# Kernel tuning notes

Hardware: AMD Instinct MI355X
Metric: run time of the kernel (lower is better)

Reference implementation:

```python
import jax, jax.numpy as jnp
import numpy as np

B = 1024      # batch
H = 512       # n_hidden
F = 32        # lstm_features
CIN = 4       # input channels
K = 30        # conv kernel
STRIDE = 6
L = 924       # input length -> T = (924-30)//6+1 = 150
KD = 40       # deconv kernel
NSTEPS = 10   # lstm_future_out
DN = ('NCH', 'OIH', 'NCH')


def setup_inputs() -> dict:
    key = jax.random.key(0)
    ks = jax.random.split(key, 14)
    s = 0.05
    rn = lambda k, shape: jax.random.normal(k, shape, jnp.float32) * s
    return dict(
        x=jax.random.normal(ks[0], (B, CIN, L), jnp.float32),
        conv_w=rn(ks[1], (F, CIN, K)), conv_b=rn(ks[2], (F,)),
        Wih0=rn(ks[3], (4 * H, F)), Whh0=rn(ks[4], (4 * H, H)),
        bih0=rn(ks[5], (4 * H,)), bhh0=rn(ks[6], (4 * H,)),
        Wih1=rn(ks[7], (4 * H, H)), Whh1=rn(ks[8], (4 * H, H)),
        bih1=rn(ks[9], (4 * H,)), bhh1=rn(ks[10], (4 * H,)),
        dec_w=rn(ks[11], (F, H)), dec_b=rn(ks[12], (F,)),
        deconv_w=rn(ks[13], (F, 1, KD)),
    )


def _cell(x, h, c, Wih, Whh, b):
    # PyTorch LSTM gate order: i, f, g, o
    g = x @ Wih.T + h @ Whh.T + b
    i, f, gg, o = jnp.split(g, 4, axis=-1)
    c = jax.nn.sigmoid(f) * c + jax.nn.sigmoid(i) * jnp.tanh(gg)
    h = jax.nn.sigmoid(o) * jnp.tanh(c)
    return h, c


def _lstm_layer(seq, Wih, Whh, b):
    # seq: [T, B, in] -> ys: [T, B, H], final (h, c)
    n = seq.shape[1]
    h0 = jnp.zeros((n, H), seq.dtype)
    c0 = jnp.zeros((n, H), seq.dtype)
    def step(carry, x):
        h, c = _cell(x, carry[0], carry[1], Wih, Whh, b)
        return (h, c), h
    (hT, cT), ys = jax.lax.scan(step, (h0, c0), seq)
    return ys, hT, cT


def _forward(x, conv_w, conv_b, Wih0, Whh0, bih0, bhh0,
             Wih1, Whh1, bih1, bhh1, dec_w, dec_b, deconv_w):
    # encoder conv: [B,4,L] -> [B,F,T]
    z = jax.lax.conv_general_dilated(x, conv_w, (STRIDE,), [(0, 0)],
                                     dimension_numbers=DN) + conv_b[None, :, None]
    z = jax.nn.relu(z)
    seq = jnp.transpose(z, (2, 0, 1))  # [T, B, F]
    b0, b1 = bih0 + bhh0, bih1 + bhh1
    s0, h0, c0 = _lstm_layer(seq, Wih0, Whh0, b0)
    s1, h1, c1 = _lstm_layer(s0, Wih1, Whh1, b1)
    out = s1 @ dec_w.T + dec_b                 # [T, B, F]
    y0 = out[-1]                               # output[-2:-1] of encoder -> last decoded step
    def dec_step(carry, _):
        y, ha, ca, hb, cb = carry
        ha, ca = _cell(y, ha, ca, Wih0, Whh0, b0)
        hb, cb = _cell(ha, hb, cb, Wih1, Whh1, b1)
        y = hb @ dec_w.T + dec_b
        return (y, ha, ca, hb, cb), y
    _, fut = jax.lax.scan(dec_step, (y0, h0, c0, h1, c1), None, length=NSTEPS)
    fut = jnp.transpose(fut, (1, 2, 0))        # [B, F, 10]
    # ConvTranspose1d (stride=1, pad=0, no bias) == cross-correlation with
    # spatially flipped, channel-swapped kernel on input padded by KD-1.
    kt = jnp.transpose(jnp.flip(deconv_w, -1), (1, 0, 2))  # [1, F, KD]
    return jax.lax.conv_general_dilated(fut, kt, (1,), [(KD - 1, KD - 1)],
                                        dimension_numbers=DN)  # [B, 1, 49]


def reference(x, conv_w, conv_b, Wih0, Whh0, bih0, bhh0,
              Wih1, Whh1, bih1, bhh1, dec_w, dec_b, deconv_w):
    return _forward(x, conv_w, conv_b, Wih0, Whh0, bih0, bhh0,
                    Wih1, Whh1, bih1, bhh1, dec_w, dec_b, deconv_w)
```

## Files before the change

kernel.cpp:

```cpp
#include <hip/hip_runtime.h>
#include <hip/hip_bf16.h>

typedef __hip_bfloat16 bf16;
typedef __attribute__((ext_vector_type(8))) short short8;
typedef __attribute__((ext_vector_type(4))) float float4v;

#define B_    1024
#define H_    512
#define G4H   2048
#define F_    32
#define CIN_  4
#define K_    30
#define STRIDE_ 6
#define L_    924
#define T_    150
#define KD_   40
#define NSTEPS_ 10
#define BH    (B_ * H_)

__device__ __forceinline__ float sigmoidf_(float x) { return 1.f / (1.f + __expf(-x)); }
__device__ __forceinline__ float tanhf_(float x)    { return 1.f - 2.f / (__expf(2.f * x) + 1.f); }
__device__ __forceinline__ float b2f_(short s) {
    return __uint_as_float(((unsigned)(unsigned short)s) << 16);
}
__device__ __forceinline__ void stwt_(bf16* p, float v) {
    union { __hip_bfloat16 b; unsigned short u; } cv;
    cv.b = __float2bfloat16(v);
    __hip_atomic_store((unsigned short*)p, cv.u, __ATOMIC_RELAXED, __HIP_MEMORY_SCOPE_AGENT);
}

__global__ __launch_bounds__(256) void cvt_kernel(const float* __restrict__ src,
                                                  bf16* __restrict__ dst, int n) {
    int i = blockIdx.x * 256 + threadIdx.x;
    if (i < n) dst[i] = __float2bfloat16(src[i]);
}

__global__ void bias_kernel(const float* __restrict__ bih0, const float* __restrict__ bhh0,
                            const float* __restrict__ bih1, const float* __restrict__ bhh1,
                            float* __restrict__ b0, float* __restrict__ b1) {
    int i = blockIdx.x * 256 + threadIdx.x;
    if (i < G4H)      b0[i] = bih0[i] + bhh0[i];
    else if (i < 2*G4H) { int j = i - G4H; b1[j] = bih1[j] + bhh1[j]; }
}

__global__ __launch_bounds__(256) void conv_kernel(
    const float* __restrict__ x, const float* __restrict__ w,
    const float* __restrict__ cb, bf16* __restrict__ seq)
{
    __shared__ float w_lds[CIN_ * K_ * F_];
    __shared__ float x_lds[CIN_ * L_];
    int tid = threadIdx.x;
    int b = blockIdx.x;
    for (int i = tid; i < CIN_ * K_ * F_; i += 256) {
        int f = i & 31, r = i >> 5;
        w_lds[r * 32 + f] = w[f * (CIN_ * K_) + r];
    }
    const float* xb = x + (size_t)b * (CIN_ * L_);
    for (int i = tid; i < CIN_ * L_; i += 256)
        x_lds[i] = xb[i];
    __syncthreads();
    int f = tid & 31, tt = tid >> 5;
    float cbf = cb[f];
    for (int t0 = 0; t0 < T_; t0 += 8) {
        int t = t0 + tt;
        if (t < T_) {
            float acc = cbf;
            #pragma unroll
            for (int c = 0; c < CIN_; ++c) {
                const float* xr = x_lds + c * L_ + t * STRIDE_;
                const float* wr = w_lds + c * K_ * 32 + f;
                #pragma unroll
                for (int k = 0; k < K_; ++k)
                    acc += xr[k] * wr[k * 32];
            }
            acc = fmaxf(acc, 0.f);
            seq[(size_t)t * (B_ * F_) + b * F_ + f] = __float2bfloat16(acc);
        }
    }
}

__device__ __forceinline__ void wait1(const int* fg, int tgt, bool inv) {
    if (tgt > 0) {
        if (threadIdx.x < 16) {
            const long long* p = (const long long*)fg + threadIdx.x;
            for (int n = 0; ; ++n) {
                long long v = __hip_atomic_load(p, __ATOMIC_RELAXED, __HIP_MEMORY_SCOPE_AGENT);
                int a = (int)v, b = (int)(v >> 32);
                if (__all(a >= tgt && b >= tgt)) break;
                if (n < 2) __builtin_amdgcn_s_sleep(2);
                else       __builtin_amdgcn_s_sleep(32);
            }
        }
        __syncthreads();
        if (inv) __builtin_amdgcn_fence(__ATOMIC_ACQUIRE, "agent");
    } else {
        __syncthreads();
    }
}

__device__ __forceinline__ void signal1(int* f, int val) {
    __syncthreads();
    if (threadIdx.x == 0) {
        __builtin_amdgcn_s_waitcnt(0);
        __hip_atomic_store(f, val, __ATOMIC_RELAXED, __HIP_MEMORY_SCOPE_AGENT);
    }
}

#define MFMA_ __builtin_amdgcn_mfma_f32_16x16x32_bf16
template<int NKS, int XSTR>
__device__ __forceinline__ void gemm_acc(
    const bf16* __restrict__ X, const short8* __restrict__ W,
    float4v (&acc)[4][4], int mrow, int quad, int lane)
{
    for (int ks = 0; ks < NKS; ++ks) {
        short8 av[4];
        #pragma unroll
        for (int ms = 0; ms < 4; ++ms)
            av[ms] = *(const short8*)(X + (size_t)(mrow + ms * 16) * XSTR
                                      + ks * 32 + quad * 8);
        #pragma unroll
        for (int g = 0; g < 4; ++g) {
            short8 bfr = W[(ks * 4 + g) * 64 + lane];
            #pragma unroll
            for (int ms = 0; ms < 4; ++ms)
                acc[ms][g] = MFMA_(av[ms], bfr, acc[ms][g], 0, 0, 0);
        }
    }
}

__device__ __forceinline__ void epilogue_(
    float4v (&acc)[4][4], float (&creg)[16], const float* __restrict__ bias,
    bf16* __restrict__ Hout, int m0, int j0, int wid, int lane)
{
    const int row16 = lane & 15;
    const int quad  = lane >> 4;
    const int j = j0 + row16;
    const float bi  = bias[j];
    const float bff = bias[H_ + j];
    const float bg  = bias[2 * H_ + j];
    const float bo  = bias[3 * H_ + j];
    #pragma unroll
    for (int ms = 0; ms < 4; ++ms) {
        #pragma unroll
        for (int r = 0; r < 4; ++r) {
            int brow = m0 + wid * 64 + ms * 16 + quad * 4 + r;
            float ig = sigmoidf_(acc[ms][0][r] + bi);
            float fg = sigmoidf_(acc[ms][1][r] + bff);
            float gg = tanhf_(acc[ms][2][r] + bg);
            float og = sigmoidf_(acc[ms][3][r] + bo);
            float cn = fg * creg[ms * 4 + r] + ig * gg;
            creg[ms * 4 + r] = cn;
            stwt_(Hout + (size_t)brow * H_ + j, og * tanhf_(cn));
        }
    }
}

struct PP {
    const bf16 *seq, *Wih0, *Whh0, *Wih1, *Whh1, *dwb;
    const float *b0, *b1, *dec_b;
    float *fut;
    bf16 *h0, *h1, *y;
    int *flags;
};

__global__ __launch_bounds__(256, 1) void lstm_persist(PP P) {
    __shared__ short8 WldsH[4096];
    __shared__ short8 WldsI[4096];

    const int bid   = blockIdx.x;
    const int gsw   = bid & 7;
    const bool isL0 = (gsw < 4);
    const int mg    = gsw & 3;
    const int jj    = bid >> 3;
    const int lb    = mg * 32 + jj;
    const int j0    = jj * 16;
    const int m0    = mg * 256;
    const int tid   = threadIdx.x;
    const int wid   = tid >> 6;
    const int lane  = tid & 63;
    const int quad  = lane >> 4;
    const int mrow  = m0 + wid * 64 + (lane & 15);

    {
        const bf16* Whh = isL0 ? P.Whh0 : P.Whh1;
        for (int i = 0; i < 16; ++i) {
            int s = tid + i * 256;
            int frag = s >> 6, ln = s & 63;
            int ks = frag >> 2, g = frag & 3;
            WldsH[s] = *(const short8*)(Whh + (size_t)(g * H_ + j0 + (ln & 15)) * H_
                                        + ks * 32 + (ln >> 4) * 8);
        }
        if (isL0) {
            if (tid < 256) {
                int frag = tid >> 6, ln = tid & 63;
                int g = frag & 3;
                WldsI[tid] = *(const short8*)(P.Wih0 + (size_t)(g * H_ + j0 + (ln & 15)) * F_
                                              + (ln >> 4) * 8);
            }
        } else {
            for (int i = 0; i < 16; ++i) {
                int s = tid + i * 256;
                int frag = s >> 6, ln = s & 63;
                int ks = frag >> 2, g = frag & 3;
                WldsI[s] = *(const short8*)(P.Wih1 + (size_t)(g * H_ + j0 + (ln & 15)) * H_
                                            + ks * 32 + (ln >> 4) * 8);
            }
        }
        __syncthreads();
    }

    float creg[16];
    #pragma unroll
    for (int i = 0; i < 16; ++i) creg[i] = 0.f;

    int* f0 = P.flags;
    int* f1 = P.flags + 128;
    int* fy = P.flags + 256;
    const int* f0g = f0 + mg * 32;
    const int* f1g = f1 + mg * 32;
    const int* fyg = fy + mg * 32;

    float4v acc[4][4];

    if (isL0) {
        for (int t = 0; t < T_; ++t) {
            wait1(f1g, t - 2, false);
            #pragma unroll
            for (int ms = 0; ms < 4; ++ms)
                #pragma unroll
                for (int g = 0; g < 4; ++g) acc[ms][g] = (float4v){0.f,0.f,0.f,0.f};
            gemm_acc<1, 32>(P.seq + (size_t)t * B_ * F_, WldsI, acc, mrow, quad, lane);
            wait1(f0g, t, true);
            gemm_acc<16, 512>(P.h0 + (size_t)((t + 2) % 3) * BH, WldsH, acc, mrow, quad, lane);
            epilogue_(acc, creg, P.b0, P.h0 + (size_t)(t % 3) * BH, m0, j0, wid, lane);
            signal1(f0 + lb, t + 1);
        }
        for (int s = 0; s <= NSTEPS_; ++s) {
            wait1(f1g, T_ + s, true);
            float yacc;
            int id = lb * 256 + tid;
            {
                int br = id >> 5, f = id & 31;
                const short8* hv = (const short8*)(P.h1 + (size_t)((T_ - 1 + s) % 3) * BH
                                                   + (size_t)br * H_);
                const short8* wv = (const short8*)(P.dwb + (size_t)f * H_);
                yacc = P.dec_b[f];
                for (int i = 0; i < H_ / 8; ++i) {
                    short8 h8 = hv[i], w8 = wv[i];
                    #pragma unroll
                    for (int k = 0; k < 8; ++k)
                        yacc += b2f_(h8[k]) * b2f_(w8[k]);
                }
            }
            if (s >= 1) wait1(f0g, T_ + s, false);
            stwt_(P.y + id, yacc);
            if (s >= 1) {
                int br = id >> 5, f = id & 31;
                P.fut[(size_t)br * (F_ * NSTEPS_) + f * NSTEPS_ + (s - 1)] = yacc;
            }
            signal1(fy + lb, s + 1);
            if (s < NSTEPS_) {
                int t = T_ + s;
                wait1(fyg, s + 1, true);
                #pragma unroll
                for (int ms = 0; ms < 4; ++ms)
                    #pragma unroll
                    for (int g = 0; g < 4; ++g) acc[ms][g] = (float4v){0.f,0.f,0.f,0.f};
                gemm_acc<1, 32>(P.y, WldsI, acc, mrow, quad, lane);
                wait1(f0g, t, true);
                gemm_acc<16, 512>(P.h0 + (size_t)((t + 2) % 3) * BH, WldsH, acc, mrow, quad, lane);
                epilogue_(acc, creg, P.b0, P.h0 + (size_t)(t % 3) * BH, m0, j0, wid, lane);
                signal1(f0 + lb, t + 1);
            }
        }
    } else {
        for (int t = 0; t < T_ + NSTEPS_; ++t) {
            wait1(f1g, t, true);
            #pragma unroll
            for (int ms = 0; ms < 4; ++ms)
                #pragma unroll
                for (int g = 0; g < 4; ++g) acc[ms][g] = (float4v){0.f,0.f,0.f,0.f};
            gemm_acc<16, 512>(P.h1 + (size_t)((t + 2) % 3) * BH, WldsH, acc, mrow, quad, lane);
            wait1(f0g, t + 1, true);
            gemm_acc<16, 512>(P.h0 + (size_t)(t % 3) * BH, WldsI, acc, mrow, quad, lane);
            epilogue_(acc, creg, P.b1, P.h1 + (size_t)(t % 3) * BH, m0, j0, wid, lane);
            signal1(f1 + lb, t + 1);
        }
    }
}

__global__ __launch_bounds__(256) void deconv_kernel(
    const float* __restrict__ fut, const float* __restrict__ dw,
    float* __restrict__ out)
{
    int idx = blockIdx.x * 256 + threadIdx.x;
    if (idx >= B_ * 49) return;
    int b = idx / 49, jj = idx % 49;
    int tlo = jj - (KD_ - 1); if (tlo < 0) tlo = 0;
    int thi = jj; if (thi > NSTEPS_ - 1) thi = NSTEPS_ - 1;
    float acc = 0.f;
    for (int f = 0; f < F_; ++f) {
        const float* fr = fut + (size_t)b * (F_ * NSTEPS_) + f * NSTEPS_;
        const float* wr = dw + f * KD_;
        for (int t = tlo; t <= thi; ++t)
            acc += fr[t] * wr[jj - t];
    }
    out[idx] = acc;
}

extern "C" void kernel_launch(void* const* d_in, const int* in_sizes, int n_in,
                              void* d_out, int out_size, void* d_ws, size_t ws_size,
                              hipStream_t stream) {
    const float* x       = (const float*)d_in[0];
    const float* conv_w  = (const float*)d_in[1];
    const float* conv_b  = (const float*)d_in[2];
    const float* Wih0f   = (const float*)d_in[3];
    const float* Whh0f   = (const float*)d_in[4];
    const float* bih0    = (const float*)d_in[5];
    const float* bhh0    = (const float*)d_in[6];
    const float* Wih1f   = (const float*)d_in[7];
    const float* Whh1f   = (const float*)d_in[8];
    const float* bih1    = (const float*)d_in[9];
    const float* bhh1    = (const float*)d_in[10];
    const float* dec_wf  = (const float*)d_in[11];
    const float* dec_b   = (const float*)d_in[12];
    const float* deconvw = (const float*)d_in[13];
    float* out = (float*)d_out;

    char* ws = (char*)d_ws;
    size_t off = 0;
    auto alloc = [&](size_t bytes) { char* p = ws + off; off = (off + bytes + 255) & ~(size_t)255; return p; };
    bf16*  seq   = (bf16*) alloc((size_t)T_ * B_ * F_ * 2);
    float* b0v   = (float*)alloc(G4H * 4);
    float* b1v   = (float*)alloc(G4H * 4);
    bf16*  h0    = (bf16*) alloc((size_t)3 * BH * 2);
    bf16*  h1    = (bf16*) alloc((size_t)3 * BH * 2);
    bf16*  y     = (bf16*) alloc((size_t)B_ * F_ * 2);
    float* fut   = (float*)alloc((size_t)B_ * F_ * NSTEPS_ * 4);
    bf16*  Wih0b = (bf16*) alloc((size_t)G4H * F_ * 2);
    bf16*  Whh0b = (bf16*) alloc((size_t)G4H * H_ * 2);
    bf16*  Wih1b = (bf16*) alloc((size_t)G4H * H_ * 2);
    bf16*  Whh1b = (bf16*) alloc((size_t)G4H * H_ * 2);
    bf16*  dec_wb= (bf16*) alloc((size_t)F_ * H_ * 2);
    int*   flags = (int*)  alloc(384 * 4);

    hipMemsetAsync(h0, 0, (size_t)3 * BH * 2, stream);
    hipMemsetAsync(h1, 0, (size_t)3 * BH * 2, stream);
    hipMemsetAsync(flags, 0, 384 * 4, stream);

    cvt_kernel<<<(G4H * F_ + 255) / 256, 256, 0, stream>>>(Wih0f, Wih0b, G4H * F_);
    cvt_kernel<<<(G4H * H_ + 255) / 256, 256, 0, stream>>>(Whh0f, Whh0b, G4H * H_);
    cvt_kernel<<<(G4H * H_ + 255) / 256, 256, 0, stream>>>(Wih1f, Wih1b, G4H * H_);
    cvt_kernel<<<(G4H * H_ + 255) / 256, 256, 0, stream>>>(Whh1f, Whh1b, G4H * H_);
    cvt_kernel<<<(F_ * H_ + 255) / 256, 256, 0, stream>>>(dec_wf, dec_wb, F_ * H_);

    bias_kernel<<<16, 256, 0, stream>>>(bih0, bhh0, bih1, bhh1, b0v, b1v);
    conv_kernel<<<B_, 256, 0, stream>>>(x, conv_w, conv_b, seq);

    PP P;
    P.seq = seq; P.Wih0 = Wih0b; P.Whh0 = Whh0b; P.Wih1 = Wih1b; P.Whh1 = Whh1b;
    P.dwb = dec_wb; P.b0 = b0v; P.b1 = b1v; P.dec_b = dec_b;
    P.fut = fut; P.h0 = h0; P.h1 = h1; P.y = y;
    P.flags = flags;

    void* args[] = { &P };
    hipError_t err = hipLaunchCooperativeKernel((const void*)lstm_persist,
                                                dim3(256), dim3(256), args, 0, stream);
    if (err != hipSuccess) {
        lstm_persist<<<256, 256, 0, stream>>>(P);
    }

    deconv_kernel<<<196, 256, 0, stream>>>(fut, deconvw, out);
}
```

Before: 5.901 ms.

## Replace acquire fences with relaxed atomic loads and merge flag waits

The per-step wait no longer issues an agent-scope acquire fence. Shared hidden-state and y buffers are instead read through relaxed agent-scope atomic 64-bit loads, which bypass stale cache lines without invalidating the whole cache. The two flag waits in layer 0 are merged into one combined poll across 32 threads, and the sleep intervals in the poll loop are shortened. The aim is to cut synchronization latency on the persistent recurrent critical path. The cost is that split 64-bit atomic loads may vectorize worse than 128-bit loads, and ordering now depends on relaxed semantics.

```diff
diff --git a/kernel.cpp b/kernel.cpp
--- a/kernel.cpp
+++ b/kernel.cpp
@@ -27,6 +27,13 @@
     union { __hip_bfloat16 b; unsigned short u; } cv;
     cv.b = __float2bfloat16(v);
     __hip_atomic_store((unsigned short*)p, cv.u, __ATOMIC_RELAXED, __HIP_MEMORY_SCOPE_AGENT);
+}
+__device__ __forceinline__ short8 lda16_(const bf16* p) {
+    const long long* q = (const long long*)p;
+    long long a = __hip_atomic_load(q,     __ATOMIC_RELAXED, __HIP_MEMORY_SCOPE_AGENT);
+    long long b = __hip_atomic_load(q + 1, __ATOMIC_RELAXED, __HIP_MEMORY_SCOPE_AGENT);
+    union { long long ll[2]; short8 s; } u; u.ll[0] = a; u.ll[1] = b;
+    return u.s;
 }
 
 __global__ __launch_bounds__(256) void cvt_kernel(const float* __restrict__ src,
@@ -79,23 +86,24 @@
     }
 }
 
-__device__ __forceinline__ void wait1(const int* fg, int tgt, bool inv) {
-    if (tgt > 0) {
-        if (threadIdx.x < 16) {
-            const long long* p = (const long long*)fg + threadIdx.x;
+__device__ __forceinline__ void waitg(const int* fa, int ta, const int* fb, int tb) {
+    const int t = threadIdx.x;
+    if (t < 32) {
+        const long long* p = nullptr; int tgt = 0;
+        if (t < 16) { if (fa && ta > 0) { p = (const long long*)fa + t;        tgt = ta; } }
+        else        { if (fb && tb > 0) { p = (const long long*)fb + (t - 16); tgt = tb; } }
+        if (__any(p != nullptr)) {
             for (int n = 0; ; ++n) {
-                long long v = __hip_atomic_load(p, __ATOMIC_RELAXED, __HIP_MEMORY_SCOPE_AGENT);
-                int a = (int)v, b = (int)(v >> 32);
-                if (__all(a >= tgt && b >= tgt)) break;
-                if (n < 2) __builtin_amdgcn_s_sleep(2);
-                else       __builtin_amdgcn_s_sleep(32);
-            }
-        }
-        __syncthreads();
-        if (inv) __builtin_amdgcn_fence(__ATOMIC_ACQUIRE, "agent");
-    } else {
-        __syncthreads();
-    }
+                long long v = p ? __hip_atomic_load(p, __ATOMIC_RELAXED, __HIP_MEMORY_SCOPE_AGENT)
+                                : 0;
+                bool ok = (p == nullptr) || ((int)v >= tgt && (int)(v >> 32) >= tgt);
+                if (__all(ok)) break;
+                if (n < 4) __builtin_amdgcn_s_sleep(1);
+                else       __builtin_amdgcn_s_sleep(8);
+            }
+        }
+    }
+    __syncthreads();
 }
 
 __device__ __forceinline__ void signal1(int* f, int val) {
@@ -107,7 +115,7 @@
 }
 
 #define MFMA_ __builtin_amdgcn_mfma_f32_16x16x32_bf16
-template<int NKS, int XSTR>
+template<int NKS, int XSTR, bool ATOM>
 __device__ __forceinline__ void gemm_acc(
     const bf16* __restrict__ X, const short8* __restrict__ W,
     float4v (&acc)[4][4], int mrow, int quad, int lane)
@@ -115,9 +123,10 @@
     for (int ks = 0; ks < NKS; ++ks) {
         short8 av[4];
         #pragma unroll
-        for (int ms = 0; ms < 4; ++ms)
-            av[ms] = *(const short8*)(X + (size_t)(mrow + ms * 16) * XSTR
-                                      + ks * 32 + quad * 8);
+        for (int ms = 0; ms < 4; ++ms) {
+            const bf16* p = X + (size_t)(mrow + ms * 16) * XSTR + ks * 32 + quad * 8;
+            av[ms] = ATOM ? lda16_(p) : *(const short8*)p;
+        }
         #pragma unroll
         for (int g = 0; g < 4; ++g) {
             short8 bfr = W[(ks * 4 + g) * 64 + lane];
@@ -224,35 +233,33 @@
 
     if (isL0) {
         for (int t = 0; t < T_; ++t) {
-            wait1(f1g, t - 2, false);
             #pragma unroll
             for (int ms = 0; ms < 4; ++ms)
                 #pragma unroll
                 for (int g = 0; g < 4; ++g) acc[ms][g] = (float4v){0.f,0.f,0.f,0.f};
-            gemm_acc<1, 32>(P.seq + (size_t)t * B_ * F_, WldsI, acc, mrow, quad, lane);
-            wait1(f0g, t, true);
-            gemm_acc<16, 512>(P.h0 + (size_t)((t + 2) % 3) * BH, WldsH, acc, mrow, quad, lane);
+            gemm_acc<1, 32, false>(P.seq + (size_t)t * B_ * F_, WldsI, acc, mrow, quad, lane);
+            waitg(f0g, t, f1g, t - 2);
+            gemm_acc<16, 512, true>(P.h0 + (size_t)((t + 2) % 3) * BH, WldsH, acc, mrow, quad, lane);
             epilogue_(acc, creg, P.b0, P.h0 + (size_t)(t % 3) * BH, m0, j0, wid, lane);
             signal1(f0 + lb, t + 1);
         }
         for (int s = 0; s <= NSTEPS_; ++s) {
-            wait1(f1g, T_ + s, true);
+            waitg(f1g, T_ + s, nullptr, 0);
             float yacc;
             int id = lb * 256 + tid;
             {
                 int br = id >> 5, f = id & 31;
-                const short8* hv = (const short8*)(P.h1 + (size_t)((T_ - 1 + s) % 3) * BH
-                                                   + (size_t)br * H_);
+                const bf16* hv = P.h1 + (size_t)((T_ - 1 + s) % 3) * BH + (size_t)br * H_;
                 const short8* wv = (const short8*)(P.dwb + (size_t)f * H_);
                 yacc = P.dec_b[f];
                 for (int i = 0; i < H_ / 8; ++i) {
-                    short8 h8 = hv[i], w8 = wv[i];
+                    short8 h8 = lda16_(hv + i * 8), w8 = wv[i];
                     #pragma unroll
                     for (int k = 0; k < 8; ++k)
                         yacc += b2f_(h8[k]) * b2f_(w8[k]);
                 }
             }
-            if (s >= 1) wait1(f0g, T_ + s, false);
+            if (s >= 1) waitg(f0g, T_ + s, nullptr, 0);
             stwt_(P.y + id, yacc);
             if (s >= 1) {
                 int br = id >> 5, f = id & 31;
@@ -261,28 +268,28 @@
             signal1(fy + lb, s + 1);
             if (s < NSTEPS_) {
                 int t = T_ + s;
-                wait1(fyg, s + 1, true);
+                waitg(fyg, s + 1, nullptr, 0);
                 #pragma unroll
                 for (int ms = 0; ms < 4; ++ms)
                     #pragma unroll
                     for (int g = 0; g < 4; ++g) acc[ms][g] = (float4v){0.f,0.f,0.f,0.f};
-                gemm_acc<1, 32>(P.y, WldsI, acc, mrow, quad, lane);
-                wait1(f0g, t, true);
-                gemm_acc<16, 512>(P.h0 + (size_t)((t + 2) % 3) * BH, WldsH, acc, mrow, quad, lane);
+                gemm_acc<1, 32, true>(P.y, WldsI, acc, mrow, quad, lane);
+                waitg(f0g, t, f1g, t - 2);
+                gemm_acc<16, 512, true>(P.h0 + (size_t)((t + 2) % 3) * BH, WldsH, acc, mrow, quad, lane);
                 epilogue_(acc, creg, P.b0, P.h0 + (size_t)(t % 3) * BH, m0, j0, wid, lane);
                 signal1(f0 + lb, t + 1);
             }
         }
     } else {
         for (int t = 0; t < T_ + NSTEPS_; ++t) {
-            wait1(f1g, t, true);
+            waitg(f1g, t, nullptr, 0);
             #pragma unroll
             for (int ms = 0; ms < 4; ++ms)
                 #pragma unroll
                 for (int g = 0; g < 4; ++g) acc[ms][g] = (float4v){0.f,0.f,0.f,0.f};
-            gemm_acc<16, 512>(P.h1 + (size_t)((t + 2) % 3) * BH, WldsH, acc, mrow, quad, lane);
-            wait1(f0g, t + 1, true);
-            gemm_acc<16, 512>(P.h0 + (size_t)(t % 3) * BH, WldsI, acc, mrow, quad, lane);
+            gemm_acc<16, 512, true>(P.h1 + (size_t)((t + 2) % 3) * BH, WldsH, acc, mrow, quad, lane);
+            waitg(f0g, t + 1, nullptr, 0);
+            gemm_acc<16, 512, true>(P.h0 + (size_t)(t % 3) * BH, WldsI, acc, mrow, quad, lane);
             epilogue_(acc, creg, P.b1, P.h1 + (size_t)(t % 3) * BH, m0, j0, wid, lane);
             signal1(f1 + lb, t + 1);
         }
```

Result: slower. 6.312 ms (+7.0%).
